# Kernel optimization log

Measured on AMD Instinct MI355X. Metric: run time of the kernel, lower is better.

Reference implementation:

```python
import jax, jax.numpy as jnp
from jax import lax
import numpy as np

MAX_REGIONS = 4          # static cap on connected components per volume
BIG = np.int32(2 ** 30)  # 'infinity' label for background in CCL
INF = jnp.float32(1e10)  # 'infinity' squared distance for EDT


def setup_inputs() -> dict:
    key = jax.random.key(0)
    B, D, H, W = 2, 96, 96, 96
    zz, yy, xx = np.meshgrid(np.arange(D), np.arange(H), np.arange(W), indexing='ij')

    def sphere(c, r):
        return (zz - c[0]) ** 2 + (yy - c[1]) ** 2 + (xx - c[2]) ** 2 <= r * r

    vols = []
    for b in range(B):  # 3 disjoint components per volume (realistic lesion GT)
        m = sphere((24 + 4 * b, 24, 24), 10) | sphere((70, 60, 30 + 6 * b), 12) | sphere((48, 72, 72), 9)
        vols.append(m)
    y = jnp.asarray(np.stack(vols)[:, None].astype(np.int32))          # (B,1,D,H,W)
    x = jax.random.normal(key, (B, 1, D, H, W), dtype=jnp.float32)     # logits
    return {"x": x, "y": y}


def _ccl(mask):
    """26-connected components (skimage/cucim default) via min-label propagation.
    Returns comp: int32 labels 1..K in raster order of first voxel (0 = bg), and K."""
    idx = jnp.arange(mask.size, dtype=jnp.int32).reshape(mask.shape)
    lab0 = jnp.where(mask, idx, BIG)

    def step(c):
        lab, _ = c
        pooled = lax.reduce_window(lab, BIG, lax.min, (3, 3, 3), (1, 1, 1), 'SAME')
        new = jnp.where(mask, pooled, BIG)
        return (new, jnp.any(new != lab))

    lab, _ = lax.while_loop(lambda c: c[1], step, (lab0, jnp.bool_(True)))
    uniq = jnp.unique(lab, size=MAX_REGIONS + 1, fill_value=BIG)  # sorted roots, padded
    K = jnp.sum(uniq < BIG).astype(jnp.int32)
    comp = jnp.searchsorted(uniq, lab.ravel()).reshape(lab.shape).astype(jnp.int32) + 1
    comp = jnp.where(mask, comp, 0)
    return comp, K


def _edt_1d(f, axis):
    """Exact 1D squared-EDT pass: out[p] = min_q (p-q)^2 + f[q]."""
    f2 = jnp.moveaxis(f, axis, 0)
    sh = f2.shape
    L = sh[0]
    f2 = f2.reshape(L, -1)
    q = jnp.arange(L, dtype=f.dtype)
    d2 = (q[:, None] - q[None, :]) ** 2                 # (L, L)
    out = jnp.min(d2[:, :, None] + f2[None, :, :], axis=1)  # (L, M)
    return jnp.moveaxis(out.reshape(sh), 0, axis)


def _edt_sq(f0):
    for ax in range(3):
        f0 = _edt_1d(f0, ax)
    return f0  # exact squared Euclidean distance to the zero set


def _voronoi(comp):
    """region_map[v] = label of nearest component (ties -> smallest label),
    mirroring the torch strict-< update loop over region labels."""
    def one(r):
        f0 = jnp.where(comp == r, jnp.float32(0.0), INF)
        return _edt_sq(f0)

    dists = lax.map(one, jnp.arange(1, MAX_REGIONS + 1, dtype=jnp.int32))  # (R,D,H,W)
    return jnp.argmin(dists, axis=0).astype(jnp.int32) + 1  # first-occurrence tie-break


def _per_volume(xb, yb):
    mask = yb > 0
    comp, K = _ccl(mask)              # multi_label: component labels 1..K
    region = _voronoi(comp)           # Voronoi regionization, labels 1..MAX_REGIONS
    seg = (region - 1).ravel()
    xs = jax.nn.sigmoid(xb).ravel()
    yl = comp.astype(jnp.float32).ravel()  # dice uses label VALUES, as in torch
    inter = jax.ops.segment_sum(xs * yl, seg, num_segments=MAX_REGIONS)
    sx = jax.ops.segment_sum(xs, seg, num_segments=MAX_REGIONS)
    sy = jax.ops.segment_sum(yl, seg, num_segments=MAX_REGIONS)
    valid = jnp.arange(MAX_REGIONS) < K
    denom = jnp.where(valid, sx + sy, jnp.float32(1.0))
    dice_r = jnp.where(valid, 2.0 * inter / denom, jnp.float32(0.0))
    mean_dice = jnp.sum(dice_r) / jnp.maximum(K, 1).astype(jnp.float32)
    return jnp.where(K == 0, jnp.float32(1.0), 1.0 - mean_dice)


def reference(x, y):
    # x: (B,1,D,H,W) logits; y: (B,1,D,H,W) int binary GT
    losses = lax.map(lambda t: _per_volume(t[0], t[1]), (x[:, 0], y[:, 0]))
    return jnp.mean(losses)
```

## Files before the change

kernel.cpp:

```cpp
#include <hip/hip_runtime.h>
#include <math.h>

#define W3 96
#define HW 9216
#define DHW 884736
#define NB 2
#define BIGL (1<<30)
#define INF10 1.0e10f
#define CAND_CAP 8192

#define A_ROOTCNT 0
#define A_ROOTS   2
#define A_CANDCNT 18
#define A_SUMS    28
#define A_TOTAL   64

__global__ void k_local(const int* __restrict__ y, int* __restrict__ lab,
                        int* __restrict__ acc, int* __restrict__ cand) {
    __shared__ int l[512];
    __shared__ int anyflag;
    int blk = blockIdx.x, t = threadIdx.x;
    if (t == 0) anyflag = 0;
    int b = blk / 1728, tb = blk - b * 1728;
    int tz = tb / 72, rr2 = tb - tz * 72, ty = rr2 / 3, tx = rr2 - ty * 3;
    int d0 = tz * 4, h0 = ty * 4, w0 = tx * 32;
    const int* yb = y + b * DHW;
    int* lb = lab + b * DHW;
    int e0 = t, e1 = t + 256;
    int dz0 = e0 >> 7, dy0 = (e0 >> 5) & 3, dx0 = e0 & 31;
    int dz1 = e1 >> 7, dy1 = (e1 >> 5) & 3, dx1 = e1 & 31;
    int g0 = (d0 + dz0) * HW + (h0 + dy0) * W3 + (w0 + dx0);
    int g1 = (d0 + dz1) * HW + (h0 + dy1) * W3 + (w0 + dx1);
    int m0 = yb[g0] > 0, m1 = yb[g1] > 0;
    l[e0] = m0 ? e0 : 0x7FFF0000;
    l[e1] = m1 ? e1 : 0x7FFF0000;
    __syncthreads();
    if (m0 | m1) anyflag = 1;
    __syncthreads();
    if (!anyflag) { lb[g0] = BIGL; lb[g1] = BIGL; return; }

    for (int it = 0; it < 7; it++) {
        int n0, n1;
        n0 = l[e0]; n1 = l[e1];
        if (m0) { if (dx0 > 0) n0 = min(n0, l[e0 - 1]);  if (dx0 < 31) n0 = min(n0, l[e0 + 1]); }
        if (m1) { if (dx1 > 0) n1 = min(n1, l[e1 - 1]);  if (dx1 < 31) n1 = min(n1, l[e1 + 1]); }
        __syncthreads();
        if (m0) l[e0] = n0;  if (m1) l[e1] = n1;
        __syncthreads();
        n0 = l[e0]; n1 = l[e1];
        if (m0) { if (dy0 > 0) n0 = min(n0, l[e0 - 32]); if (dy0 < 3) n0 = min(n0, l[e0 + 32]); }
        if (m1) { if (dy1 > 0) n1 = min(n1, l[e1 - 32]); if (dy1 < 3) n1 = min(n1, l[e1 + 32]); }
        __syncthreads();
        if (m0) l[e0] = n0;  if (m1) l[e1] = n1;
        __syncthreads();
        n0 = l[e0]; n1 = l[e1];
        if (m0) { if (dz0 > 0) n0 = min(n0, l[e0 - 128]); if (dz0 < 3) n0 = min(n0, l[e0 + 128]); }
        if (m1) { if (dz1 > 0) n1 = min(n1, l[e1 - 128]); if (dz1 < 3) n1 = min(n1, l[e1 + 128]); }
        __syncthreads();
        if (m0) l[e0] = n0;  if (m1) l[e1] = n1;
        __syncthreads();
        n0 = m0 ? l[l[e0]] : 0;  n1 = m1 ? l[l[e1]] : 0;
        __syncthreads();
        if (m0) l[e0] = n0;  if (m1) l[e1] = n1;
        __syncthreads();
    }
    if (m0) {
        int r = l[e0]; while (l[r] != r) r = l[r];
        lb[g0] = (d0 + (r >> 7)) * HW + (h0 + ((r >> 5) & 3)) * W3 + (w0 + (r & 31));
        if (r == e0) { int c = atomicAdd(&acc[A_CANDCNT + b], 1);
                       if (c < CAND_CAP) cand[b * CAND_CAP + c] = g0; }
    } else lb[g0] = BIGL;
    if (m1) {
        int r = l[e1]; while (l[r] != r) r = l[r];
        lb[g1] = (d0 + (r >> 7)) * HW + (h0 + ((r >> 5) & 3)) * W3 + (w0 + (r & 31));
        if (r == e1) { int c = atomicAdd(&acc[A_CANDCNT + b], 1);
                       if (c < CAND_CAP) cand[b * CAND_CAP + c] = g1; }
    } else lb[g1] = BIGL;
}

__device__ __forceinline__ int ufind(int* __restrict__ lb, int v) {
    int p = lb[v];
    if (p == v) return p;
    int root = p;
    while (true) { int pp = lb[root]; if (pp == root) break; root = pp; }
    if (root < p) atomicMin(&lb[v], root);
    return root;
}

__device__ void unite(int* __restrict__ lb, int a, int b) {
    while (true) {
        a = ufind(lb, a); b = ufind(lb, b);
        if (a == b) return;
        int mn = min(a, b), mx = max(a, b);
        int old = atomicMin(&lb[mx], mn);
        if (old == mx) return;
        a = old; b = mn;
    }
}

__constant__ int c_offs[13][3] = {
    {-1,-1,-1},{-1,-1,0},{-1,-1,1},
    {-1, 0,-1},{-1, 0,0},{-1, 0,1},
    {-1, 1,-1},{-1, 1,0},{-1, 1,1},
    { 0,-1,-1},{ 0,-1,0},{ 0,-1,1},
    { 0, 0,-1}};

__global__ void k_bmerge(const int* __restrict__ y, int* __restrict__ lab) {
    int i = blockIdx.x * blockDim.x + threadIdx.x;
    if (i >= NB * DHW) return;
    int b = i / DHW, v = i - b * DHW;
    int d = v / HW; int rem = v - d * HW; int h = rem / W3; int w = rem - h * W3;
    int fz = ((d & 3) == 0), fy = ((h & 3) == 0), fx = ((w & 31) == 0);
    if (!(fz | fy | fx)) return;
    if (y[i] <= 0) return;
    const int* yb = y + b * DHW;
    int* lb = lab + b * DHW;
    #pragma unroll
    for (int k = 0; k < 13; k++) {
        int oz = c_offs[k][0], oy = c_offs[k][1], ox = c_offs[k][2];
        int cross = (fz && oz < 0) || (fy && oy < 0) || (fx && ox < 0);
        if (!cross) continue;
        int dd = d + oz, hh = h + oy, ww = w + ox;
        if ((unsigned)dd >= W3 || (unsigned)hh >= W3 || (unsigned)ww >= W3) continue;
        int u = dd * HW + hh * W3 + ww;
        if (yb[u] > 0) unite(lb, v, u);
    }
}

__global__ void k_collect(const int* __restrict__ lab, int* __restrict__ acc,
                          const int* __restrict__ cand) {
    int t = threadIdx.x;
    for (int b = 0; b < NB; b++) {
        int cnt = acc[A_CANDCNT + b]; if (cnt > CAND_CAP) cnt = CAND_CAP;
        const int* lb = lab + b * DHW;
        for (int i = t; i < cnt; i += 256) {
            int g = cand[b * CAND_CAP + i];
            if (lb[g] == g) {
                int c = atomicAdd(&acc[A_ROOTCNT + b], 1);
                if (c < 8) acc[A_ROOTS + b * 8 + c] = g;
            }
        }
    }
}

__device__ __forceinline__ int gfind(const int* __restrict__ lb, int t) {
    while (true) { int p = lb[t]; if (p == t) break; t = p; }
    return t;
}

__device__ __forceinline__ int rankc2(int t, const int rt[8], int n) {
    int c = 1;
    #pragma unroll
    for (int p = 0; p < 8; p++) c += (p < n && rt[p] < t) ? 1 : 0;
    return c;
}

__global__ void k_keys(const int* __restrict__ lab, const int* __restrict__ acc,
                       float* __restrict__ keys) {
    int i = blockIdx.x * blockDim.x + threadIdx.x;
    if (i >= NB * DHW) return;
    int b = i / DHW;
    int n = acc[A_ROOTCNT + b]; if (n > 8) n = 8;
    int rt[8];
    #pragma unroll
    for (int p = 0; p < 8; p++) rt[p] = acc[A_ROOTS + b * 8 + p];
    int tv = lab[i];
    float val = INF10;
    if (tv != BIGL) val = 0.125f * (float)rankc2(gfind(lab + b * DHW, tv), rt, n);
    keys[i] = val;
}

__global__ __launch_bounds__(384) void k_pedtD(const float* __restrict__ fin,
                                               float* __restrict__ out) {
    __shared__ float A[96 * 101];
    int blk = blockIdx.x;
    int b = blk / 384, r = blk % 384;
    int h = r / 4, d0 = (r % 4) * 24;
    int t = threadIdx.x;
    size_t vbase = (size_t)b * DHW;
    #pragma unroll
    for (int m = 0; m < 24; m++) {
        int e = t + 384 * m;
        int dd = e / 96, w2 = e - dd * 96;
        A[dd * 101 + w2] = fin[vbase + (size_t)dd * HW + h * W3 + w2];
    }
    __syncthreads();
    int w = t % 96, dg = t / 96;
    int dbase = d0 + dg * 6;
    float best[6], dq[6];
    #pragma unroll
    for (int k = 0; k < 6; k++) { best[k] = 3.9e37f; dq[k] = (float)(dbase + k); }
    for (int q = 0; q < 96; q++) {
        float val = A[q * 101 + w];
        #pragma unroll
        for (int k = 0; k < 6; k++) {
            best[k] = fminf(best[k], fmaf(dq[k], dq[k], val));
            dq[k] -= 1.0f;
        }
    }
    #pragma unroll
    for (int k = 0; k < 6; k++)
        out[vbase + (size_t)(dbase + k) * HW + h * W3 + w] = best[k];
}

__device__ __forceinline__ float wred(float v) {
    v += __shfl_xor(v, 32, 64);
    v += __shfl_xor(v, 16, 64);
    v += __shfl_xor(v, 8, 64);
    v += __shfl_xor(v, 4, 64);
    v += __shfl_xor(v, 2, 64);
    v += __shfl_xor(v, 1, 64);
    return v;
}

__global__ __launch_bounds__(384) void k_pedtHW_acc(const float* __restrict__ fin,
                                                    const float* __restrict__ x,
                                                    const int* __restrict__ lab,
                                                    int* __restrict__ acc) {
    __shared__ float A[96 * 101];
    __shared__ float Bf[24 * 101];
    __shared__ float red[6][12];
    int blk = blockIdx.x;
    int b = blk / 384, r = blk % 384;
    int d = r / 4, h0 = (r % 4) * 24;
    size_t sbase = (size_t)b * DHW + (size_t)d * HW;
    const int* lb = lab + (size_t)b * DHW;
    int t = threadIdx.x;
    int n = acc[A_ROOTCNT + b]; if (n > 8) n = 8;
    int rt[8];
    #pragma unroll
    for (int p = 0; p < 8; p++) rt[p] = acc[A_ROOTS + b * 8 + p];
    #pragma unroll
    for (int m = 0; m < 24; m++) {
        int e = t + 384 * m;
        int hh = e / 96, w2 = e - hh * 96;
        A[hh * 101 + w2] = fin[sbase + e];
    }
    __syncthreads();
    {
        int w = t % 96, hg = t / 96;
        int hb = h0 + hg * 6;
        float best[6], dq[6];
        #pragma unroll
        for (int k = 0; k < 6; k++) { best[k] = 3.9e37f; dq[k] = (float)(hb + k); }
        for (int q = 0; q < 96; q++) {
            float val = A[q * 101 + w];
            #pragma unroll
            for (int k = 0; k < 6; k++) {
                best[k] = fminf(best[k], fmaf(dq[k], dq[k], val));
                dq[k] -= 1.0f;
            }
        }
        #pragma unroll
        for (int k = 0; k < 6; k++) Bf[(hg * 6 + k) * 101 + w] = best[k];
    }
    __syncthreads();
    {
        int rr = t % 24, cg = t / 24;
        int wb = cg * 6;
        float best[6], dq[6];
        #pragma unroll
        for (int k = 0; k < 6; k++) { best[k] = 3.9e37f; dq[k] = (float)(wb + k); }
        for (int q = 0; q < 96; q++) {
            float val = Bf[rr * 101 + q];
            #pragma unroll
            for (int k = 0; k < 6; k++) {
                best[k] = fminf(best[k], fmaf(dq[k], dq[k], val));
                dq[k] -= 1.0f;
            }
        }
        #pragma unroll
        for (int k = 0; k < 6; k++) A[rr * 101 + wb + k] = best[k];
    }
    __syncthreads();
    float aA[4] = {0,0,0,0}, aM[4] = {0,0,0,0}, aC[4] = {0,0,0,0};
    size_t qbase = sbase + (size_t)h0 * W3;
    #pragma unroll
    for (int m = 0; m < 6; m++) {
        int e = t + 384 * m;
        int rr = e / 96, w2 = e - rr * 96;
        float key = A[rr * 101 + w2];
        int key8 = (int)(key * 8.0f);
        int seg = (key8 & 7) - 1;
        seg = (seg < 0) ? 0 : ((seg > 3) ? 3 : seg);
        float xs = 1.0f / (1.0f + expf(-x[qbase + e]));
        int tv = lab[qbase + e];
        int c = 0;
        if (tv != BIGL) c = rankc2(gfind(lb, tv), rt, n);
        #pragma unroll
        for (int s = 0; s < 4; s++) {
            aA[s] += (seg == s) ? xs : 0.0f;
            aM[s] += (c == s + 1) ? xs : 0.0f;
            aC[s] += (c == s + 1) ? 1.0f : 0.0f;
        }
    }
    #pragma unroll
    for (int s = 0; s < 4; s++) { aA[s] = wred(aA[s]); aM[s] = wred(aM[s]); aC[s] = wred(aC[s]); }
    int lane = t & 63, wv = t >> 6;
    if (lane == 0) {
        #pragma unroll
        for (int s = 0; s < 4; s++) {
            red[wv][s] = aA[s]; red[wv][4 + s] = aM[s]; red[wv][8 + s] = aC[s];
        }
    }
    __syncthreads();
    if (t < 12) {
        float v = red[0][t] + red[1][t] + red[2][t] + red[3][t] + red[4][t] + red[5][t];
        atomicAdd((float*)&acc[A_SUMS + b * 12 + t], v);
    }
}

__global__ void k_loss(const int* __restrict__ acc, float* __restrict__ out) {
    if (threadIdx.x == 0 && blockIdx.x == 0) {
        const float* sums = (const float*)&acc[A_SUMS];
        float total = 0.0f;
        for (int b = 0; b < NB; b++) {
            int n = acc[A_ROOTCNT + b];
            int K = (n > 5) ? 5 : n;
            float s = 0.0f;
            for (int r = 0; r < 4; r++) {
                if (r < K) {
                    float A = sums[b * 12 + r];
                    float M = sums[b * 12 + 4 + r];
                    float C = sums[b * 12 + 8 + r];
                    float inter = (float)(r + 1) * M;
                    float sy = (float)(r + 1) * C;
                    s += 2.0f * inter / (A + sy);
                }
            }
            float Kf = (float)(K > 0 ? K : 1);
            total += (K == 0) ? 1.0f : (1.0f - s / Kf);
        }
        out[0] = total / (float)NB;
    }
}

extern "C" void kernel_launch(void* const* d_in, const int* in_sizes, int n_in,
                              void* d_out, int out_size, void* d_ws, size_t ws_size,
                              hipStream_t stream) {
    const float* x = (const float*)d_in[0];
    const int*   y = (const int*)d_in[1];
    float* out = (float*)d_out;

    char* ws = (char*)d_ws;
    int*   acc  = (int*)ws;
    int*   cand = (int*)(ws + 1024);
    int*   lab  = (int*)(ws + 1024 + CAND_CAP * NB * 4);
    float* kA   = (float*)((char*)lab + (size_t)NB * DHW * 4);
    float* kB   = (float*)((char*)kA + (size_t)NB * DHW * 4);

    dim3 blk(256);
    dim3 g1((NB * DHW) / 256);
    dim3 gl(NB * 1728);
    dim3 gq(NB * 96 * 4);
    dim3 b384(384);

    hipMemsetAsync(acc, 0, 256, stream);
    k_local<<<gl, blk, 0, stream>>>(y, lab, acc, cand);
    k_bmerge<<<g1, blk, 0, stream>>>(y, lab);
    k_collect<<<1, blk, 0, stream>>>(lab, acc, cand);
    k_keys<<<g1, blk, 0, stream>>>(lab, acc, kA);
    k_pedtD<<<gq, b384, 0, stream>>>(kA, kB);
    k_pedtHW_acc<<<gq, b384, 0, stream>>>(kB, x, lab, acc);
    k_loss<<<1, 64, 0, stream>>>(acc, out);
}
```

Baseline: 162.9 us.

## Fuse key computation into D-pass EDT and derive component labels from EDT keys

Removes the separate k_keys kernel: the D-axis EDT pass now computes each voxel's key directly from the union-find labels and root ranks while loading its shared tile. The final HW pass no longer reloads labels or runs union-find. It recovers the component id from the fractional part of the propagated key, since a zero-distance voxel keeps its own rank encoding. This saves one launch plus a full-volume write and read of the key buffer and a second label traversal. It relies on the key encoding staying exact for foreground voxels.

```diff
diff --git a/kernel.cpp b/kernel.cpp
--- a/kernel.cpp
+++ b/kernel.cpp
@@ -155,34 +155,28 @@
     return c;
 }
 
-__global__ void k_keys(const int* __restrict__ lab, const int* __restrict__ acc,
-                       float* __restrict__ keys) {
-    int i = blockIdx.x * blockDim.x + threadIdx.x;
-    if (i >= NB * DHW) return;
-    int b = i / DHW;
-    int n = acc[A_ROOTCNT + b]; if (n > 8) n = 8;
-    int rt[8];
-    #pragma unroll
-    for (int p = 0; p < 8; p++) rt[p] = acc[A_ROOTS + b * 8 + p];
-    int tv = lab[i];
-    float val = INF10;
-    if (tv != BIGL) val = 0.125f * (float)rankc2(gfind(lab + b * DHW, tv), rt, n);
-    keys[i] = val;
-}
-
-__global__ __launch_bounds__(384) void k_pedtD(const float* __restrict__ fin,
+__global__ __launch_bounds__(384) void k_pedtD(const int* __restrict__ lab,
+                                               const int* __restrict__ acc,
                                                float* __restrict__ out) {
     __shared__ float A[96 * 101];
     int blk = blockIdx.x;
     int b = blk / 384, r = blk % 384;
-    int h = r / 4, d0 = (r % 4) * 24;
+    int h = r >> 2, d0 = (r & 3) * 24;
+    const int* lb = lab + (size_t)b * DHW;
     int t = threadIdx.x;
+    int n = acc[A_ROOTCNT + b]; if (n > 8) n = 8;
+    int rt[8];
+    #pragma unroll
+    for (int p = 0; p < 8; p++) rt[p] = acc[A_ROOTS + b * 8 + p];
     size_t vbase = (size_t)b * DHW;
     #pragma unroll
     for (int m = 0; m < 24; m++) {
         int e = t + 384 * m;
         int dd = e / 96, w2 = e - dd * 96;
-        A[dd * 101 + w2] = fin[vbase + (size_t)dd * HW + h * W3 + w2];
+        int tv = lb[dd * HW + h * W3 + w2];
+        float val = INF10;
+        if (tv != BIGL) val = 0.125f * (float)rankc2(gfind(lb, tv), rt, n);
+        A[dd * 101 + w2] = val;
     }
     __syncthreads();
     int w = t % 96, dg = t / 96;
@@ -215,21 +209,15 @@
 
 __global__ __launch_bounds__(384) void k_pedtHW_acc(const float* __restrict__ fin,
                                                     const float* __restrict__ x,
-                                                    const int* __restrict__ lab,
                                                     int* __restrict__ acc) {
     __shared__ float A[96 * 101];
     __shared__ float Bf[24 * 101];
     __shared__ float red[6][12];
     int blk = blockIdx.x;
     int b = blk / 384, r = blk % 384;
-    int d = r / 4, h0 = (r % 4) * 24;
+    int d = r >> 2, h0 = (r & 3) * 24;
     size_t sbase = (size_t)b * DHW + (size_t)d * HW;
-    const int* lb = lab + (size_t)b * DHW;
     int t = threadIdx.x;
-    int n = acc[A_ROOTCNT + b]; if (n > 8) n = 8;
-    int rt[8];
-    #pragma unroll
-    for (int p = 0; p < 8; p++) rt[p] = acc[A_ROOTS + b * 8 + p];
     #pragma unroll
     for (int m = 0; m < 24; m++) {
         int e = t + 384 * m;
@@ -283,10 +271,8 @@
         int key8 = (int)(key * 8.0f);
         int seg = (key8 & 7) - 1;
         seg = (seg < 0) ? 0 : ((seg > 3) ? 3 : seg);
+        int c = (key8 < 8) ? (seg + 1) : 0;
         float xs = 1.0f / (1.0f + expf(-x[qbase + e]));
-        int tv = lab[qbase + e];
-        int c = 0;
-        if (tv != BIGL) c = rankc2(gfind(lb, tv), rt, n);
         #pragma unroll
         for (int s = 0; s < 4; s++) {
             aA[s] += (seg == s) ? xs : 0.0f;
@@ -346,8 +332,7 @@
     int*   acc  = (int*)ws;
     int*   cand = (int*)(ws + 1024);
     int*   lab  = (int*)(ws + 1024 + CAND_CAP * NB * 4);
-    float* kA   = (float*)((char*)lab + (size_t)NB * DHW * 4);
-    float* kB   = (float*)((char*)kA + (size_t)NB * DHW * 4);
+    float* kB   = (float*)((char*)lab + (size_t)NB * DHW * 4);
 
     dim3 blk(256);
     dim3 g1((NB * DHW) / 256);
@@ -359,8 +344,7 @@
     k_local<<<gl, blk, 0, stream>>>(y, lab, acc, cand);
     k_bmerge<<<g1, blk, 0, stream>>>(y, lab);
     k_collect<<<1, blk, 0, stream>>>(lab, acc, cand);
-    k_keys<<<g1, blk, 0, stream>>>(lab, acc, kA);
-    k_pedtD<<<gq, b384, 0, stream>>>(kA, kB);
-    k_pedtHW_acc<<<gq, b384, 0, stream>>>(kB, x, lab, acc);
+    k_pedtD<<<gq, b384, 0, stream>>>(lab, acc, kB);
+    k_pedtHW_acc<<<gq, b384, 0, stream>>>(kB, x, acc);
     k_loss<<<1, 64, 0, stream>>>(acc, out);
 }
```

Result: faster. 159.1 us (-2.3%).
